# Kernel optimization log

Measured on AMD Instinct MI355X. Metric: run time of the kernel, lower is better.

The kernel has to match this reference:

```python
import jax, jax.numpy as jnp
import numpy as np

OBS = 4096      # flattened observation size (hardcoded in down_sampler)
ENC = 1024      # encoding_size
LAT = 512       # policy_latent_size
ACT = 3         # action_space_n
B = 4096        # batch
NMAX = 8        # max neighbors (padded ragged dim)


def setup_inputs() -> dict:
    key = jax.random.key(0)
    ks = jax.random.split(key, 16)

    def w(i, shape, fan_in):
        return jax.random.normal(ks[i], shape, jnp.float32) * (1.0 / np.sqrt(fan_in))

    return {
        "observation": jax.random.normal(ks[0], (B, OBS), jnp.float32),
        "neighbors": jax.random.normal(ks[1], (B, NMAX, LAT), jnp.float32),
        "neighbor_counts": jax.random.randint(ks[2], (B,), 0, 9, jnp.int32),
        # down_sampler: Linear(4096, ENC) + ReLU
        "W_ds": w(3, (ENC, OBS), OBS), "b_ds": jnp.zeros((ENC,), jnp.float32),
        # policy: Linear(ENC, LAT) + ReLU
        "W_pol": w(4, (LAT, ENC), ENC), "b_pol": jnp.zeros((LAT,), jnp.float32),
        # v_net: Linear(ENC, 1) + Tanh
        "W_v": w(5, (1, ENC), ENC), "b_v": jnp.zeros((1,), jnp.float32),
        # GRUCell(LAT, LAT): weight_ih [3L, L], weight_hh [3L, L]
        "W_ih": w(6, (3 * LAT, LAT), LAT), "b_ih": jnp.zeros((3 * LAT,), jnp.float32),
        "W_hh": w(7, (3 * LAT, LAT), LAT), "b_hh": jnp.zeros((3 * LAT,), jnp.float32),
        # to_probs: Linear(LAT, ACT) + ReLU + Softmax
        "W_pr": w(8, (ACT, LAT), LAT), "b_pr": jnp.zeros((ACT,), jnp.float32),
    }


def _gru_cell(x, h, W_ih, b_ih, W_hh, b_hh):
    # PyTorch GRUCell semantics; gates ordered (r, z, n)
    gi = x @ W_ih.T + b_ih          # [B, 3L]
    gh = h @ W_hh.T + b_hh          # [B, 3L]
    i_r, i_z, i_n = jnp.split(gi, 3, axis=-1)
    h_r, h_z, h_n = jnp.split(gh, 3, axis=-1)
    r = jax.nn.sigmoid(i_r + h_r)
    z = jax.nn.sigmoid(i_z + h_z)
    n = jnp.tanh(i_n + r * h_n)
    return (1.0 - z) * n + z * h


def reference(observation, neighbors, neighbor_counts,
              W_ds, b_ds, W_pol, b_pol, W_v, b_v,
              W_ih, b_ih, W_hh, b_hh, W_pr, b_pr):
    # step 0: forward_initial
    enc = jax.nn.relu(observation @ W_ds.T + b_ds)        # [B, ENC]
    pol = jax.nn.relu(enc @ W_pol.T + b_pol)              # [B, LAT]
    state_vals = jnp.tanh(enc @ W_v.T + b_v)              # [B, 1]

    # step 1: forward_communicate -- ragged GRU recurrence over padded neighbors
    xs = jnp.swapaxes(neighbors, 0, 1)                    # [NMAX, B, LAT]
    ts = jnp.arange(NMAX)

    def step(h, xt):
        x, t = xt
        h_new = _gru_cell(x, h, W_ih, b_ih, W_hh, b_hh)
        valid = (t < neighbor_counts)[:, None]            # mask padded neighbor slots
        return jnp.where(valid, h_new, h), None

    h, _ = jax.lax.scan(step, pol, (xs, ts))              # [B, LAT]

    # step 2: forward_probs
    probs = jax.nn.softmax(jax.nn.relu(h @ W_pr.T + b_pr), axis=-1)  # [B, ACT]
    return probs, state_vals
```

## Files before the change

### kernel.cpp

```cpp
#include <hip/hip_runtime.h>
#include <hip/hip_bf16.h>

typedef __attribute__((ext_vector_type(8))) short short8;
typedef __attribute__((ext_vector_type(4))) float floatx4;

__device__ __forceinline__ ushort f2bf(float x) {
    unsigned u = __float_as_uint(x);
    unsigned r = (u + 0x7fffu + ((u >> 16) & 1u)) >> 16;
    return (ushort)r;
}
__device__ __forceinline__ float bf2f(ushort h) {
    return __uint_as_float(((unsigned)h) << 16);
}
__device__ __forceinline__ float fast_sigmoid(float x) {
    return 1.0f / (1.0f + __expf(-x));
}
__device__ __forceinline__ float fast_tanh(float x) {
    x = fminf(fmaxf(x, -15.0f), 15.0f);
    float e = __expf(2.0f * x);
    return (e - 1.0f) / (e + 1.0f);
}
__device__ __forceinline__ void load_lds16(const void* g, void* l) {
    __builtin_amdgcn_global_load_lds(
        (__attribute__((address_space(1))) void*)(g),
        (__attribute__((address_space(3))) void*)(l),
        16, 0, 0);
}

__device__ __forceinline__ void stage_unit(const ushort* grow0, int ld, ushort* lds_unit) {
    const int lane = threadIdx.x & 63;
    const int r = lane >> 3;
    const int c = (lane & 7) ^ r;
    load_lds16(grow0 + (size_t)r * ld + c * 8, lds_unit);
}
__device__ __forceinline__ short8 lds_read8(const ushort* buf, int R, int c_el) {
    const int idx = ((R >> 3) << 9) + ((R & 7) << 6) + ((((c_el >> 3) ^ (R & 7))) << 3);
    return *(const short8*)(buf + idx);
}

__global__ __launch_bounds__(256) void cvt_f32_bf16(const float* __restrict__ src,
                                                    ushort* __restrict__ dst, int n4) {
    int i = blockIdx.x * blockDim.x + threadIdx.x;
    if (i >= n4) return;
    const float4 v = ((const float4*)src)[i];
    ushort4 o;
    o.x = f2bf(v.x); o.y = f2bf(v.y); o.z = f2bf(v.z); o.w = f2bf(v.w);
    ((ushort4*)dst)[i] = o;
}

__global__ __launch_bounds__(256) void sort_by_cnt(const int* __restrict__ cnt,
                                                   int* __restrict__ perm,
                                                   int* __restrict__ inv,
                                                   int* __restrict__ nact) {
    __shared__ int h[9];
    __shared__ int cur[9];
    const int tid = threadIdx.x;
    if (tid < 9) h[tid] = 0;
    __syncthreads();
    for (int i = tid; i < 4096; i += 256) atomicAdd(&h[cnt[i]], 1);
    __syncthreads();
    if (tid == 0) {
        int off = 0;
        for (int c = 8; c >= 0; --c) { cur[c] = off; off += h[c]; }
        for (int t = 0; t < 8; ++t) {
            int n = 0;
            for (int c = t + 1; c <= 8; ++c) n += h[c];
            nact[t] = n;
        }
    }
    __syncthreads();
    for (int i = tid; i < 4096; i += 256) {
        const int c = cnt[i];
        const int p = atomicAdd(&cur[c], 1);
        perm[p] = i;
        inv[i] = p;
    }
}

template <int MODE, int BN, int KSPLIT, bool MAP>
__global__ __launch_bounds__(256, 2) void gemm64(
    const ushort* __restrict__ A, int lda,
    const ushort* __restrict__ B, int ldb,
    const float* __restrict__ bias,
    const int* __restrict__ row_map,
    ushort* __restrict__ Cb, float* __restrict__ Cf, int ldc,
    int K, size_t part_stride) {
    __shared__ __attribute__((aligned(16))) ushort sA[64 * 64];
    __shared__ __attribute__((aligned(16))) ushort sB[BN * 64];

    constexpr int NJ = (BN + 63) / 64;
    constexpr int UB = BN / 32;

    const int tid = threadIdx.x;
    const int lane = tid & 63;
    const int w = tid >> 6;
    const int m0 = blockIdx.y * 64;
    const int n0 = blockIdx.x * BN;
    const int wn = w * (16 * NJ);
    const int nl = lane & 15;

    const int Kper = K / KSPLIT;
    const int kbase = (KSPLIT > 1) ? blockIdx.z * Kper : 0;
    if (MODE == 3) Cf += (size_t)blockIdx.z * part_stride;

    floatx4 acc[4][NJ] = {};

    for (int k0 = kbase; k0 < kbase + Kper; k0 += 64) {
#pragma unroll
        for (int u = 0; u < 2; ++u) {
            const int ua = w * 2 + u;
            stage_unit(A + (size_t)(m0 + ua * 8) * lda + k0, lda, &sA[ua * 512]);
        }
#pragma unroll
        for (int u = 0; u < UB; ++u) {
            const int ub = w * UB + u;
            stage_unit(B + (size_t)(n0 + ub * 8) * ldb + k0, ldb, &sB[ub * 512]);
        }
        __syncthreads();
#pragma unroll
        for (int kk = 0; kk < 2; ++kk) {
            const int cb = kk * 32 + (lane >> 4) * 8;
            short8 a[4], b[NJ];
#pragma unroll
            for (int i = 0; i < 4; ++i) a[i] = lds_read8(sA, i * 16 + nl, cb);
#pragma unroll
            for (int j = 0; j < NJ; ++j) b[j] = lds_read8(sB, wn + j * 16 + nl, cb);
#pragma unroll
            for (int i = 0; i < 4; ++i)
#pragma unroll
                for (int j = 0; j < NJ; ++j)
                    acc[i][j] = __builtin_amdgcn_mfma_f32_16x16x32_bf16(a[i], b[j], acc[i][j], 0, 0, 0);
        }
        __syncthreads();
    }

    const int ml = (lane >> 4) * 4;
#pragma unroll
    for (int j = 0; j < NJ; ++j) {
        const int n = n0 + wn + j * 16 + nl;
        float bv = 0.0f;
        if (MODE == 2) bv = bias[n];
#pragma unroll
        for (int i = 0; i < 4; ++i) {
            const int mbase = m0 + i * 16 + ml;
#pragma unroll
            for (int r = 0; r < 4; ++r) {
                float v = acc[i][j][r];
                const int mr = mbase + r;
                const int orow = MAP ? row_map[mr] : mr;
                const size_t off = (size_t)orow * ldc + n;
                if (MODE == 2) {
                    v += bv; v = fmaxf(v, 0.0f);
                    Cb[off] = f2bf(v);
                    Cf[off] = v;
                } else {
                    Cf[off] = v;
                }
            }
        }
    }
}

__global__ __launch_bounds__(256) void combine_relu(const float* __restrict__ p0,
                                                    const float* __restrict__ p1,
                                                    const float* __restrict__ bias,
                                                    ushort* __restrict__ ob, int n4) {
    int i = blockIdx.x * blockDim.x + threadIdx.x;
    if (i >= n4) return;
    const float4 a = ((const float4*)p0)[i];
    const float4 b = ((const float4*)p1)[i];
    const int col = (i * 4) & 1023;
    const float4 bs = *(const float4*)(bias + col);
    ushort4 o;
    o.x = f2bf(fmaxf(a.x + b.x + bs.x, 0.f));
    o.y = f2bf(fmaxf(a.y + b.y + bs.y, 0.f));
    o.z = f2bf(fmaxf(a.z + b.z + bs.z, 0.f));
    o.w = f2bf(fmaxf(a.w + b.w + bs.w, 0.f));
    ((ushort4*)ob)[i] = o;
}

__global__ __launch_bounds__(256, 2) void gru_step(
    const ushort* __restrict__ Xall,
    const ushort* __restrict__ Hin,
    const ushort* __restrict__ Wih,
    const ushort* __restrict__ Whh,
    const float* __restrict__ bih, const float* __restrict__ bhh,
    const int* __restrict__ perm, const int* __restrict__ nact,
    float* __restrict__ hf, ushort* __restrict__ Hout, int t) {
    __shared__ __attribute__((aligned(16))) ushort sX[64 * 64];
    __shared__ __attribute__((aligned(16))) ushort sH[64 * 64];
    __shared__ __attribute__((aligned(16))) ushort sBih[192 * 64];
    __shared__ __attribute__((aligned(16))) ushort sBhh[192 * 64];

    const int tid = threadIdx.x;
    const int lane = tid & 63;
    const int w = tid >> 6;
    const int s = blockIdx.x;
    const int m0 = blockIdx.y * 64;
    const int na = nact[t];

    if (m0 >= na) {
        const int rr = tid >> 2;
        const size_t base = (size_t)(m0 + rr) * 512 + s * 64;
        const uint4* src = (const uint4*)(Hin + base);
        uint4* dst = (uint4*)(Hout + base);
        const int cc = (tid & 3) * 2;
        dst[cc] = src[cc];
        dst[cc + 1] = src[cc + 1];
        return;
    }

    const int nl = lane & 15;
    const int ml = (lane >> 4) * 4;
    const int col = s * 64 + w * 16 + nl;

    const int r = lane >> 3;
    const int c = (lane & 7) ^ r;
    const ushort* X = Xall + t * 512;
    const ushort* xb[2];
    const ushort* hbp[2];
#pragma unroll
    for (int u = 0; u < 2; ++u) {
        const int srow = m0 + (w * 2 + u) * 8 + r;
        const int orig = perm[srow];
        xb[u] = X + (size_t)orig * 4096 + c * 8;
        hbp[u] = Hin + (size_t)srow * 512 + c * 8;
    }
    const ushort* wi[6];
    const ushort* wh[6];
#pragma unroll
    for (int j = 0; j < 6; ++j) {
        const int u = w * 6 + j;
        const int grow = (u >> 3) * 512 + s * 64 + (u & 7) * 8 + r;
        wi[j] = Wih + (size_t)grow * 512 + c * 8;
        wh[j] = Whh + (size_t)grow * 512 + c * 8;
    }

    floatx4 accr[4], accz[4], accn[4], acch[4];
    {
        const float br_ = bih[col] + bhh[col];
        const float bz_ = bih[512 + col] + bhh[512 + col];
        const float bn_i = bih[1024 + col];
        const float bn_h = bhh[1024 + col];
        const floatx4 vr = {br_, br_, br_, br_};
        const floatx4 vz = {bz_, bz_, bz_, bz_};
        const floatx4 vi = {bn_i, bn_i, bn_i, bn_i};
        const floatx4 vh = {bn_h, bn_h, bn_h, bn_h};
#pragma unroll
        for (int i = 0; i < 4; ++i) { accr[i] = vr; accz[i] = vz; accn[i] = vi; acch[i] = vh; }
    }

    for (int k0 = 0; k0 < 512; k0 += 64) {
#pragma unroll
        for (int u = 0; u < 2; ++u) {
            const int ua = w * 2 + u;
            load_lds16(xb[u] + k0, &sX[ua * 512]);
            load_lds16(hbp[u] + k0, &sH[ua * 512]);
        }
#pragma unroll
        for (int j = 0; j < 6; ++j) {
            const int u = w * 6 + j;
            load_lds16(wi[j] + k0, &sBih[u * 512]);
            load_lds16(wh[j] + k0, &sBhh[u * 512]);
        }
        __syncthreads();
#pragma unroll
        for (int kk = 0; kk < 2; ++kk) {
            const int cb = kk * 32 + (lane >> 4) * 8;
            short8 ax[4], ah[4];
#pragma unroll
            for (int i = 0; i < 4; ++i) {
                ax[i] = lds_read8(sX, i * 16 + nl, cb);
                ah[i] = lds_read8(sH, i * 16 + nl, cb);
            }
            const short8 bir = lds_read8(sBih, w * 16 + nl, cb);
            const short8 biz = lds_read8(sBih, 64 + w * 16 + nl, cb);
            const short8 bin = lds_read8(sBih, 128 + w * 16 + nl, cb);
            const short8 bhr = lds_read8(sBhh, w * 16 + nl, cb);
            const short8 bhz = lds_read8(sBhh, 64 + w * 16 + nl, cb);
            const short8 bhn = lds_read8(sBhh, 128 + w * 16 + nl, cb);
#pragma unroll
            for (int i = 0; i < 4; ++i) {
                accr[i] = __builtin_amdgcn_mfma_f32_16x16x32_bf16(ax[i], bir, accr[i], 0, 0, 0);
                accr[i] = __builtin_amdgcn_mfma_f32_16x16x32_bf16(ah[i], bhr, accr[i], 0, 0, 0);
                accz[i] = __builtin_amdgcn_mfma_f32_16x16x32_bf16(ax[i], biz, accz[i], 0, 0, 0);
                accz[i] = __builtin_amdgcn_mfma_f32_16x16x32_bf16(ah[i], bhz, accz[i], 0, 0, 0);
                accn[i] = __builtin_amdgcn_mfma_f32_16x16x32_bf16(ax[i], bin, accn[i], 0, 0, 0);
                acch[i] = __builtin_amdgcn_mfma_f32_16x16x32_bf16(ah[i], bhn, acch[i], 0, 0, 0);
            }
        }
        __syncthreads();
    }

    const bool full = (m0 + 64 <= na);
#pragma unroll
    for (int i = 0; i < 4; ++i) {
#pragma unroll
        for (int r4 = 0; r4 < 4; ++r4) {
            const int lr = i * 16 + ml + r4;
            const int row = m0 + lr;
            const float rg = fast_sigmoid(accr[i][r4]);
            const float zg = fast_sigmoid(accz[i][r4]);
            const float ng = fast_tanh(accn[i][r4] + rg * acch[i][r4]);
            const size_t off = (size_t)row * 512 + col;
            const float ho = hf[off];
            const bool act = full || (row < na);
            const float hv = act ? ((1.0f - zg) * ng + zg * ho) : ho;
            hf[off] = hv;
            Hout[off] = f2bf(hv);
        }
    }
}

__global__ __launch_bounds__(256) void v_kernel(const ushort* __restrict__ enc,
                                                const float* __restrict__ Wv,
                                                const float* __restrict__ bv,
                                                float* __restrict__ out) {
    const int row = blockIdx.x * 4 + (threadIdx.x >> 6);
    const int lane = threadIdx.x & 63;
    const ushort* e = enc + (size_t)row * 1024;
    float s = 0.0f;
#pragma unroll
    for (int i = 0; i < 16; ++i) {
        int k = lane + i * 64;
        s += bf2f(e[k]) * Wv[k];
    }
#pragma unroll
    for (int off = 32; off; off >>= 1) s += __shfl_down(s, off, 64);
    if (lane == 0) out[row] = fast_tanh(s + bv[0]);
}

__global__ __launch_bounds__(256) void probs_kernel(const float* __restrict__ h,
                                                    const float* __restrict__ Wpr,
                                                    const float* __restrict__ bpr,
                                                    const int* __restrict__ perm,
                                                    float* __restrict__ out) {
    const int srow = blockIdx.x * 4 + (threadIdx.x >> 6);
    const int lane = threadIdx.x & 63;
    const float* hr = h + (size_t)srow * 512;
    float p0 = 0.f, p1 = 0.f, p2 = 0.f;
#pragma unroll
    for (int i = 0; i < 8; ++i) {
        int k = lane + i * 64;
        float x = hr[k];
        p0 += x * Wpr[k];
        p1 += x * Wpr[512 + k];
        p2 += x * Wpr[1024 + k];
    }
#pragma unroll
    for (int off = 32; off; off >>= 1) {
        p0 += __shfl_down(p0, off, 64);
        p1 += __shfl_down(p1, off, 64);
        p2 += __shfl_down(p2, off, 64);
    }
    if (lane == 0) {
        const int orow = perm[srow];
        p0 = fmaxf(p0 + bpr[0], 0.f);
        p1 = fmaxf(p1 + bpr[1], 0.f);
        p2 = fmaxf(p2 + bpr[2], 0.f);
        float m = fmaxf(p0, fmaxf(p1, p2));
        float e0 = __expf(p0 - m), e1 = __expf(p1 - m), e2 = __expf(p2 - m);
        float inv = 1.0f / (e0 + e1 + e2);
        out[orow * 3 + 0] = e0 * inv;
        out[orow * 3 + 1] = e1 * inv;
        out[orow * 3 + 2] = e2 * inv;
    }
}

extern "C" void kernel_launch(void* const* d_in, const int* in_sizes, int n_in,
                              void* d_out, int out_size, void* d_ws, size_t ws_size,
                              hipStream_t stream) {
    const float* obs   = (const float*)d_in[0];
    const float* nbr   = (const float*)d_in[1];
    const int*   cnt   = (const int*)d_in[2];
    const float* W_ds  = (const float*)d_in[3];
    const float* b_ds  = (const float*)d_in[4];
    const float* W_pol = (const float*)d_in[5];
    const float* b_pol = (const float*)d_in[6];
    const float* W_v   = (const float*)d_in[7];
    const float* b_v   = (const float*)d_in[8];
    const float* W_ih  = (const float*)d_in[9];
    const float* b_ih  = (const float*)d_in[10];
    const float* W_hh  = (const float*)d_in[11];
    const float* b_hh  = (const float*)d_in[12];
    const float* W_pr  = (const float*)d_in[13];
    const float* b_pr  = (const float*)d_in[14];
    float* out = (float*)d_out;

    ushort* obs_b  = (ushort*)d_ws;
    ushort* Wds_b  = obs_b + 16777216;
    ushort* Wpol_b = Wds_b + 4194304;
    ushort* Wih_b  = Wpol_b + 524288;
    ushort* Whh_b  = Wih_b + 786432;
    ushort* enc_b  = Whh_b + 786432;
    ushort* h_b0   = enc_b + 4194304;
    ushort* h_b1   = h_b0 + 2097152;
    float*  h_f    = (float*)(h_b1 + 2097152);
    float*  part   = h_f + 2097152;
    ushort* nbr_b  = (ushort*)part;
    int*    perm   = (int*)(part + 8388608);
    int*    inv    = perm + 4096;
    int*    nact   = inv + 4096;

    sort_by_cnt<<<1, 256, 0, stream>>>(cnt, perm, inv, nact);

    cvt_f32_bf16<<<16384, 256, 0, stream>>>(obs, obs_b, 4194304);
    cvt_f32_bf16<<<4096, 256, 0, stream>>>(W_ds, Wds_b, 1048576);
    cvt_f32_bf16<<<512, 256, 0, stream>>>(W_pol, Wpol_b, 131072);
    cvt_f32_bf16<<<768, 256, 0, stream>>>(W_ih, Wih_b, 196608);
    cvt_f32_bf16<<<768, 256, 0, stream>>>(W_hh, Whh_b, 196608);

    gemm64<3, 128, 2, false><<<dim3(8, 64, 2), 256, 0, stream>>>(
        obs_b, 4096, Wds_b, 4096, nullptr, nullptr, nullptr, part, 1024, 4096, 4194304);
    combine_relu<<<4096, 256, 0, stream>>>(part, part + 4194304, b_ds, enc_b, 1048576);

    cvt_f32_bf16<<<16384, 256, 0, stream>>>(nbr, nbr_b, 4194304);

    gemm64<2, 64, 1, true><<<dim3(8, 64, 1), 256, 0, stream>>>(
        enc_b, 1024, Wpol_b, 1024, b_pol, inv, h_b0, h_f, 512, 1024, 0);

    v_kernel<<<1024, 256, 0, stream>>>(enc_b, W_v, b_v, out + 12288);

    for (int t = 0; t < 8; ++t) {
        const ushort* hin = (t & 1) ? h_b1 : h_b0;
        ushort* hout = (t & 1) ? h_b0 : h_b1;
        gru_step<<<dim3(8, 64), 256, 0, stream>>>(nbr_b, hin, Wih_b, Whh_b,
                                                  b_ih, b_hh, perm, nact, h_f, hout, t);
    }

    probs_kernel<<<1024, 256, 0, stream>>>(h_f, W_pr, b_pr, perm, out);
}
```

Measured before the change: 445.6 us.

## Double-buffer LDS and read weight fragments directly from global in GEMM and GRU

Adds a new down-sampler GEMM kernel with 128x256 tiles that double-buffers only the A tile in LDS and loads B (weight) fragments straight from global memory into registers. The GRU step kernel is changed the same way: X/H tiles are double-buffered with one barrier per K step, and W_ih/W_hh fragments are loaded per lane from global instead of being staged in LDS. The goal is to overlap loads with MFMA, cut barriers, and shrink LDS use. The cost is uncoalesced global weight reads that now depend on the cache, plus higher register pressure from the 8x4 accumulator tile.

```diff
diff --git a/kernel.cpp b/kernel.cpp
--- a/kernel.cpp
+++ b/kernel.cpp
@@ -27,15 +27,15 @@
         16, 0, 0);
 }
 
+__device__ __forceinline__ short8 lds_read8(const ushort* buf, int R, int c_el) {
+    const int idx = ((R >> 3) << 9) + ((R & 7) << 6) + ((((c_el >> 3) ^ (R & 7))) << 3);
+    return *(const short8*)(buf + idx);
+}
 __device__ __forceinline__ void stage_unit(const ushort* grow0, int ld, ushort* lds_unit) {
     const int lane = threadIdx.x & 63;
     const int r = lane >> 3;
     const int c = (lane & 7) ^ r;
     load_lds16(grow0 + (size_t)r * ld + c * 8, lds_unit);
-}
-__device__ __forceinline__ short8 lds_read8(const ushort* buf, int R, int c_el) {
-    const int idx = ((R >> 3) << 9) + ((R & 7) << 6) + ((((c_el >> 3) ^ (R & 7))) << 3);
-    return *(const short8*)(buf + idx);
 }
 
 __global__ __launch_bounds__(256) void cvt_f32_bf16(const float* __restrict__ src,
@@ -77,14 +77,92 @@
     }
 }
 
-template <int MODE, int BN, int KSPLIT, bool MAP>
+template <int KSPLIT>
+__global__ __launch_bounds__(256, 2) void gemm_bigm(
+    const ushort* __restrict__ A, int lda,
+    const ushort* __restrict__ B, int ldb,
+    float* __restrict__ Cf, int ldc, int K, size_t part_stride) {
+    __shared__ __attribute__((aligned(16))) ushort sA[2][128 * 64];
+
+    const int tid = threadIdx.x;
+    const int lane = tid & 63;
+    const int w = tid >> 6;
+    const int m0 = blockIdx.y * 128;
+    const int n0 = blockIdx.x * 256;
+    const int nl = lane & 15;
+    const int wcol = (lane >> 4) * 8;
+
+    const int Kper = K / KSPLIT;
+    const int kbase = blockIdx.z * Kper;
+    Cf += (size_t)blockIdx.z * part_stride;
+
+    const int r = lane >> 3;
+    const int c = (lane & 7) ^ r;
+    const ushort* ab[4];
+#pragma unroll
+    for (int u = 0; u < 4; ++u) {
+        const int ua = w * 4 + u;
+        ab[u] = A + (size_t)(m0 + ua * 8 + r) * lda + kbase + c * 8;
+    }
+    const ushort* bp[4];
+#pragma unroll
+    for (int j = 0; j < 4; ++j)
+        bp[j] = B + (size_t)(n0 + w * 64 + j * 16 + nl) * ldb + kbase + wcol;
+
+    floatx4 acc[8][4] = {};
+
+#pragma unroll
+    for (int u = 0; u < 4; ++u) load_lds16(ab[u], &sA[0][(w * 4 + u) * 512]);
+
+    const int iters = Kper / 64;
+    for (int it = 0; it < iters; ++it) {
+        const int cur = it & 1;
+        __syncthreads();
+        if (it + 1 < iters) {
+            const int kn = (it + 1) * 64;
+#pragma unroll
+            for (int u = 0; u < 4; ++u) load_lds16(ab[u] + kn, &sA[cur ^ 1][(w * 4 + u) * 512]);
+        }
+        const int k0 = it * 64;
+#pragma unroll
+        for (int kk = 0; kk < 2; ++kk) {
+            const int kc = k0 + kk * 32;
+            short8 b[4];
+#pragma unroll
+            for (int j = 0; j < 4; ++j) b[j] = *(const short8*)(bp[j] + kc);
+            const int cb = kk * 32 + wcol;
+            short8 a[8];
+#pragma unroll
+            for (int i = 0; i < 8; ++i) a[i] = lds_read8(&sA[cur][0], i * 16 + nl, cb);
+#pragma unroll
+            for (int i = 0; i < 8; ++i)
+#pragma unroll
+                for (int j = 0; j < 4; ++j)
+                    acc[i][j] = __builtin_amdgcn_mfma_f32_16x16x32_bf16(a[i], b[j], acc[i][j], 0, 0, 0);
+        }
+    }
+
+    const int ml = (lane >> 4) * 4;
+#pragma unroll
+    for (int j = 0; j < 4; ++j) {
+        const int n = n0 + w * 64 + j * 16 + nl;
+#pragma unroll
+        for (int i = 0; i < 8; ++i) {
+            const int mbase = m0 + i * 16 + ml;
+#pragma unroll
+            for (int r4 = 0; r4 < 4; ++r4)
+                Cf[(size_t)(mbase + r4) * ldc + n] = acc[i][j][r4];
+        }
+    }
+}
+
+template <int MODE, int BN, bool MAP>
 __global__ __launch_bounds__(256, 2) void gemm64(
     const ushort* __restrict__ A, int lda,
     const ushort* __restrict__ B, int ldb,
     const float* __restrict__ bias,
     const int* __restrict__ row_map,
-    ushort* __restrict__ Cb, float* __restrict__ Cf, int ldc,
-    int K, size_t part_stride) {
+    ushort* __restrict__ Cb, float* __restrict__ Cf, int ldc, int K) {
     __shared__ __attribute__((aligned(16))) ushort sA[64 * 64];
     __shared__ __attribute__((aligned(16))) ushort sB[BN * 64];
 
@@ -99,13 +177,9 @@
     const int wn = w * (16 * NJ);
     const int nl = lane & 15;
 
-    const int Kper = K / KSPLIT;
-    const int kbase = (KSPLIT > 1) ? blockIdx.z * Kper : 0;
-    if (MODE == 3) Cf += (size_t)blockIdx.z * part_stride;
-
     floatx4 acc[4][NJ] = {};
 
-    for (int k0 = kbase; k0 < kbase + Kper; k0 += 64) {
+    for (int k0 = 0; k0 < K; k0 += 64) {
 #pragma unroll
         for (int u = 0; u < 2; ++u) {
             const int ua = w * 2 + u;
@@ -138,8 +212,7 @@
 #pragma unroll
     for (int j = 0; j < NJ; ++j) {
         const int n = n0 + wn + j * 16 + nl;
-        float bv = 0.0f;
-        if (MODE == 2) bv = bias[n];
+        const float bv = bias[n];
 #pragma unroll
         for (int i = 0; i < 4; ++i) {
             const int mbase = m0 + i * 16 + ml;
@@ -149,13 +222,9 @@
                 const int mr = mbase + r;
                 const int orow = MAP ? row_map[mr] : mr;
                 const size_t off = (size_t)orow * ldc + n;
-                if (MODE == 2) {
-                    v += bv; v = fmaxf(v, 0.0f);
-                    Cb[off] = f2bf(v);
-                    Cf[off] = v;
-                } else {
-                    Cf[off] = v;
-                }
+                v += bv; v = fmaxf(v, 0.0f);
+                Cb[off] = f2bf(v);
+                Cf[off] = v;
             }
         }
     }
@@ -187,10 +256,8 @@
     const float* __restrict__ bih, const float* __restrict__ bhh,
     const int* __restrict__ perm, const int* __restrict__ nact,
     float* __restrict__ hf, ushort* __restrict__ Hout, int t) {
-    __shared__ __attribute__((aligned(16))) ushort sX[64 * 64];
-    __shared__ __attribute__((aligned(16))) ushort sH[64 * 64];
-    __shared__ __attribute__((aligned(16))) ushort sBih[192 * 64];
-    __shared__ __attribute__((aligned(16))) ushort sBhh[192 * 64];
+    __shared__ __attribute__((aligned(16))) ushort sX[2][64 * 64];
+    __shared__ __attribute__((aligned(16))) ushort sH[2][64 * 64];
 
     const int tid = threadIdx.x;
     const int lane = tid & 63;
@@ -212,6 +279,7 @@
 
     const int nl = lane & 15;
     const int ml = (lane >> 4) * 4;
+    const int wcol = (lane >> 4) * 8;
     const int col = s * 64 + w * 16 + nl;
 
     const int r = lane >> 3;
@@ -222,74 +290,80 @@
 #pragma unroll
     for (int u = 0; u < 2; ++u) {
         const int srow = m0 + (w * 2 + u) * 8 + r;
-        const int orig = perm[srow];
-        xb[u] = X + (size_t)orig * 4096 + c * 8;
+        xb[u] = X + (size_t)perm[srow] * 4096 + c * 8;
         hbp[u] = Hin + (size_t)srow * 512 + c * 8;
     }
-    const ushort* wi[6];
-    const ushort* wh[6];
-#pragma unroll
-    for (int j = 0; j < 6; ++j) {
-        const int u = w * 6 + j;
-        const int grow = (u >> 3) * 512 + s * 64 + (u & 7) * 8 + r;
-        wi[j] = Wih + (size_t)grow * 512 + c * 8;
-        wh[j] = Whh + (size_t)grow * 512 + c * 8;
-    }
+    const ushort* pir = Wih + (size_t)col * 512 + wcol;
+    const ushort* piz = Wih + (size_t)(512 + col) * 512 + wcol;
+    const ushort* pin = Wih + (size_t)(1024 + col) * 512 + wcol;
+    const ushort* phr = Whh + (size_t)col * 512 + wcol;
+    const ushort* phz = Whh + (size_t)(512 + col) * 512 + wcol;
+    const ushort* phn = Whh + (size_t)(1024 + col) * 512 + wcol;
 
     floatx4 accr[4], accz[4], accn[4], acch[4];
     {
         const float br_ = bih[col] + bhh[col];
         const float bz_ = bih[512 + col] + bhh[512 + col];
-        const float bn_i = bih[1024 + col];
-        const float bn_h = bhh[1024 + col];
+        const float bni = bih[1024 + col];
+        const float bnh = bhh[1024 + col];
         const floatx4 vr = {br_, br_, br_, br_};
         const floatx4 vz = {bz_, bz_, bz_, bz_};
-        const floatx4 vi = {bn_i, bn_i, bn_i, bn_i};
-        const floatx4 vh = {bn_h, bn_h, bn_h, bn_h};
+        const floatx4 vi = {bni, bni, bni, bni};
+        const floatx4 vh = {bnh, bnh, bnh, bnh};
 #pragma unroll
         for (int i = 0; i < 4; ++i) { accr[i] = vr; accz[i] = vz; accn[i] = vi; acch[i] = vh; }
     }
 
-    for (int k0 = 0; k0 < 512; k0 += 64) {
-#pragma unroll
-        for (int u = 0; u < 2; ++u) {
-            const int ua = w * 2 + u;
-            load_lds16(xb[u] + k0, &sX[ua * 512]);
-            load_lds16(hbp[u] + k0, &sH[ua * 512]);
-        }
-#pragma unroll
-        for (int j = 0; j < 6; ++j) {
-            const int u = w * 6 + j;
-            load_lds16(wi[j] + k0, &sBih[u * 512]);
-            load_lds16(wh[j] + k0, &sBhh[u * 512]);
-        }
+#pragma unroll
+    for (int u = 0; u < 2; ++u) {
+        const int ua = w * 2 + u;
+        load_lds16(xb[u], &sX[0][ua * 512]);
+        load_lds16(hbp[u], &sH[0][ua * 512]);
+    }
+
+    for (int it = 0; it < 8; ++it) {
+        const int cur = it & 1;
         __syncthreads();
+        if (it < 7) {
+            const int kn = (it + 1) * 64;
+#pragma unroll
+            for (int u = 0; u < 2; ++u) {
+                const int ua = w * 2 + u;
+                load_lds16(xb[u] + kn, &sX[cur ^ 1][ua * 512]);
+                load_lds16(hbp[u] + kn, &sH[cur ^ 1][ua * 512]);
+            }
+        }
+        const int k0 = it * 64;
+        short8 wf[12];
 #pragma unroll
         for (int kk = 0; kk < 2; ++kk) {
-            const int cb = kk * 32 + (lane >> 4) * 8;
+            const int kc = k0 + kk * 32;
+            wf[kk * 6 + 0] = *(const short8*)(pir + kc);
+            wf[kk * 6 + 1] = *(const short8*)(piz + kc);
+            wf[kk * 6 + 2] = *(const short8*)(pin + kc);
+            wf[kk * 6 + 3] = *(const short8*)(phr + kc);
+            wf[kk * 6 + 4] = *(const short8*)(phz + kc);
+            wf[kk * 6 + 5] = *(const short8*)(phn + kc);
+        }
+#pragma unroll
+        for (int kk = 0; kk < 2; ++kk) {
+            const int cb = kk * 32 + wcol;
             short8 ax[4], ah[4];
 #pragma unroll
             for (int i = 0; i < 4; ++i) {
-                ax[i] = lds_read8(sX, i * 16 + nl, cb);
-                ah[i] = lds_read8(sH, i * 16 + nl, cb);
+                ax[i] = lds_read8(&sX[cur][0], i * 16 + nl, cb);
+                ah[i] = lds_read8(&sH[cur][0], i * 16 + nl, cb);
             }
-            const short8 bir = lds_read8(sBih, w * 16 + nl, cb);
-            const short8 biz = lds_read8(sBih, 64 + w * 16 + nl, cb);
-            const short8 bin = lds_read8(sBih, 128 + w * 16 + nl, cb);
-            const short8 bhr = lds_read8(sBhh, w * 16 + nl, cb);
-            const short8 bhz = lds_read8(sBhh, 64 + w * 16 + nl, cb);
-            const short8 bhn = lds_read8(sBhh, 128 + w * 16 + nl, cb);
 #pragma unroll
             for (int i = 0; i < 4; ++i) {
-                accr[i] = __builtin_amdgcn_mfma_f32_16x16x32_bf16(ax[i], bir, accr[i], 0, 0, 0);
-                accr[i] = __builtin_amdgcn_mfma_f32_16x16x32_bf16(ah[i], bhr, accr[i], 0, 0, 0);
-                accz[i] = __builtin_amdgcn_mfma_f32_16x16x32_bf16(ax[i], biz, accz[i], 0, 0, 0);
-                accz[i] = __builtin_amdgcn_mfma_f32_16x16x32_bf16(ah[i], bhz, accz[i], 0, 0, 0);
-                accn[i] = __builtin_amdgcn_mfma_f32_16x16x32_bf16(ax[i], bin, accn[i], 0, 0, 0);
-                acch[i] = __builtin_amdgcn_mfma_f32_16x16x32_bf16(ah[i], bhn, acch[i], 0, 0, 0);
+                accr[i] = __builtin_amdgcn_mfma_f32_16x16x32_bf16(ax[i], wf[kk * 6 + 0], accr[i], 0, 0, 0);
+                accr[i] = __builtin_amdgcn_mfma_f32_16x16x32_bf16(ah[i], wf[kk * 6 + 3], accr[i], 0, 0, 0);
+                accz[i] = __builtin_amdgcn_mfma_f32_16x16x32_bf16(ax[i], wf[kk * 6 + 1], accz[i], 0, 0, 0);
+                accz[i] = __builtin_amdgcn_mfma_f32_16x16x32_bf16(ah[i], wf[kk * 6 + 4], accz[i], 0, 0, 0);
+                accn[i] = __builtin_amdgcn_mfma_f32_16x16x32_bf16(ax[i], wf[kk * 6 + 2], accn[i], 0, 0, 0);
+                acch[i] = __builtin_amdgcn_mfma_f32_16x16x32_bf16(ah[i], wf[kk * 6 + 5], acch[i], 0, 0, 0);
             }
         }
-        __syncthreads();
     }
 
     const bool full = (m0 + 64 <= na);
@@ -297,8 +371,7 @@
     for (int i = 0; i < 4; ++i) {
 #pragma unroll
         for (int r4 = 0; r4 < 4; ++r4) {
-            const int lr = i * 16 + ml + r4;
-            const int row = m0 + lr;
+            const int row = m0 + i * 16 + ml + r4;
             const float rg = fast_sigmoid(accr[i][r4]);
             const float zg = fast_sigmoid(accz[i][r4]);
             const float ng = fast_tanh(accn[i][r4] + rg * acch[i][r4]);
@@ -410,14 +483,14 @@
     cvt_f32_bf16<<<768, 256, 0, stream>>>(W_ih, Wih_b, 196608);
     cvt_f32_bf16<<<768, 256, 0, stream>>>(W_hh, Whh_b, 196608);
 
-    gemm64<3, 128, 2, false><<<dim3(8, 64, 2), 256, 0, stream>>>(
-        obs_b, 4096, Wds_b, 4096, nullptr, nullptr, nullptr, part, 1024, 4096, 4194304);
+    gemm_bigm<2><<<dim3(4, 32, 2), 256, 0, stream>>>(
+        obs_b, 4096, Wds_b, 4096, part, 1024, 4096, 4194304);
     combine_relu<<<4096, 256, 0, stream>>>(part, part + 4194304, b_ds, enc_b, 1048576);
 
     cvt_f32_bf16<<<16384, 256, 0, stream>>>(nbr, nbr_b, 4194304);
 
-    gemm64<2, 64, 1, true><<<dim3(8, 64, 1), 256, 0, stream>>>(
-        enc_b, 1024, Wpol_b, 1024, b_pol, inv, h_b0, h_f, 512, 1024, 0);
+    gemm64<2, 64, true><<<dim3(8, 64), 256, 0, stream>>>(
+        enc_b, 1024, Wpol_b, 1024, b_pol, inv, h_b0, h_f, 512, 1024);
 
     v_kernel<<<1024, 256, 0, stream>>>(enc_b, W_v, b_v, out + 12288);
 
```

Measured after the change: 529.0 us. 18.7% more time.

## Retile GRU step to 128-row tiles with double-buffered LDS and register weights

Applied to the files above, without the earlier changes.

The GRU step kernel now covers 128 batch rows per block instead of 64, with the grid reordered to (M tiles, column slices). X and H tiles are double-buffered in LDS so the next K chunk's global-to-LDS copies overlap the current MFMAs, and one barrier per iteration replaces two. Weight fragments are read straight from global memory into registers rather than staged through LDS. This is meant to amortise the weight traffic over more rows and hide load latency. In exchange it launches fewer blocks, roughly doubles accumulator registers (launch bound lowered to one block per SIMD set), and exposes global-load latency on the weight reads.

```diff
diff --git a/kernel.cpp b/kernel.cpp
--- a/kernel.cpp
+++ b/kernel.cpp
@@ -27,15 +27,15 @@
         16, 0, 0);
 }
 
+__device__ __forceinline__ short8 lds_read8(const ushort* buf, int R, int c_el) {
+    const int idx = ((R >> 3) << 9) + ((R & 7) << 6) + ((((c_el >> 3) ^ (R & 7))) << 3);
+    return *(const short8*)(buf + idx);
+}
 __device__ __forceinline__ void stage_unit(const ushort* grow0, int ld, ushort* lds_unit) {
     const int lane = threadIdx.x & 63;
     const int r = lane >> 3;
     const int c = (lane & 7) ^ r;
     load_lds16(grow0 + (size_t)r * ld + c * 8, lds_unit);
-}
-__device__ __forceinline__ short8 lds_read8(const ushort* buf, int R, int c_el) {
-    const int idx = ((R >> 3) << 9) + ((R & 7) << 6) + ((((c_el >> 3) ^ (R & 7))) << 3);
-    return *(const short8*)(buf + idx);
 }
 
 __global__ __launch_bounds__(256) void cvt_f32_bf16(const float* __restrict__ src,
@@ -179,7 +179,7 @@
     ((ushort4*)ob)[i] = o;
 }
 
-__global__ __launch_bounds__(256, 2) void gru_step(
+__global__ __launch_bounds__(256, 1) void gru_step(
     const ushort* __restrict__ Xall,
     const ushort* __restrict__ Hin,
     const ushort* __restrict__ Wih,
@@ -187,100 +187,102 @@
     const float* __restrict__ bih, const float* __restrict__ bhh,
     const int* __restrict__ perm, const int* __restrict__ nact,
     float* __restrict__ hf, ushort* __restrict__ Hout, int t) {
-    __shared__ __attribute__((aligned(16))) ushort sX[64 * 64];
-    __shared__ __attribute__((aligned(16))) ushort sH[64 * 64];
-    __shared__ __attribute__((aligned(16))) ushort sBih[192 * 64];
-    __shared__ __attribute__((aligned(16))) ushort sBhh[192 * 64];
+    __shared__ __attribute__((aligned(16))) ushort sX[2][128 * 64];
+    __shared__ __attribute__((aligned(16))) ushort sH[2][128 * 64];
 
     const int tid = threadIdx.x;
     const int lane = tid & 63;
     const int w = tid >> 6;
-    const int s = blockIdx.x;
-    const int m0 = blockIdx.y * 64;
+    const int m0 = blockIdx.x * 128;
+    const int s = blockIdx.y;
     const int na = nact[t];
 
     if (m0 >= na) {
-        const int rr = tid >> 2;
+        const int rr = tid >> 1;
         const size_t base = (size_t)(m0 + rr) * 512 + s * 64;
         const uint4* src = (const uint4*)(Hin + base);
         uint4* dst = (uint4*)(Hout + base);
-        const int cc = (tid & 3) * 2;
-        dst[cc] = src[cc];
-        dst[cc + 1] = src[cc + 1];
+        const int cc = (tid & 1) * 4;
+#pragma unroll
+        for (int q = 0; q < 4; ++q) dst[cc + q] = src[cc + q];
         return;
     }
 
     const int nl = lane & 15;
     const int ml = (lane >> 4) * 4;
+    const int wcol = (lane >> 4) * 8;
     const int col = s * 64 + w * 16 + nl;
 
     const int r = lane >> 3;
     const int c = (lane & 7) ^ r;
     const ushort* X = Xall + t * 512;
-    const ushort* xb[2];
-    const ushort* hbp[2];
-#pragma unroll
-    for (int u = 0; u < 2; ++u) {
-        const int srow = m0 + (w * 2 + u) * 8 + r;
-        const int orig = perm[srow];
-        xb[u] = X + (size_t)orig * 4096 + c * 8;
-        hbp[u] = Hin + (size_t)srow * 512 + c * 8;
-    }
-    const ushort* wi[6];
-    const ushort* wh[6];
-#pragma unroll
-    for (int j = 0; j < 6; ++j) {
-        const int u = w * 6 + j;
-        const int grow = (u >> 3) * 512 + s * 64 + (u & 7) * 8 + r;
-        wi[j] = Wih + (size_t)grow * 512 + c * 8;
-        wh[j] = Whh + (size_t)grow * 512 + c * 8;
-    }
-
-    floatx4 accr[4], accz[4], accn[4], acch[4];
+    const ushort* xb[4];
+    const ushort* hb[4];
+#pragma unroll
+    for (int u = 0; u < 4; ++u) {
+        const int srow = m0 + (w * 4 + u) * 8 + r;
+        xb[u] = X + (size_t)perm[srow] * 4096 + c * 8;
+        hb[u] = Hin + (size_t)srow * 512 + c * 8;
+    }
+    const ushort* pir = Wih + (size_t)col * 512 + wcol;
+    const ushort* piz = Wih + (size_t)(512 + col) * 512 + wcol;
+    const ushort* pin = Wih + (size_t)(1024 + col) * 512 + wcol;
+    const ushort* phr = Whh + (size_t)col * 512 + wcol;
+    const ushort* phz = Whh + (size_t)(512 + col) * 512 + wcol;
+    const ushort* phn = Whh + (size_t)(1024 + col) * 512 + wcol;
+
+    floatx4 accr[8], accz[8], accn[8], acch[8];
     {
         const float br_ = bih[col] + bhh[col];
         const float bz_ = bih[512 + col] + bhh[512 + col];
-        const float bn_i = bih[1024 + col];
-        const float bn_h = bhh[1024 + col];
+        const float bni = bih[1024 + col];
+        const float bnh = bhh[1024 + col];
         const floatx4 vr = {br_, br_, br_, br_};
         const floatx4 vz = {bz_, bz_, bz_, bz_};
-        const floatx4 vi = {bn_i, bn_i, bn_i, bn_i};
-        const floatx4 vh = {bn_h, bn_h, bn_h, bn_h};
-#pragma unroll
-        for (int i = 0; i < 4; ++i) { accr[i] = vr; accz[i] = vz; accn[i] = vi; acch[i] = vh; }
-    }
-
-    for (int k0 = 0; k0 < 512; k0 += 64) {
-#pragma unroll
-        for (int u = 0; u < 2; ++u) {
-            const int ua = w * 2 + u;
-            load_lds16(xb[u] + k0, &sX[ua * 512]);
-            load_lds16(hbp[u] + k0, &sH[ua * 512]);
-        }
-#pragma unroll
-        for (int j = 0; j < 6; ++j) {
-            const int u = w * 6 + j;
-            load_lds16(wi[j] + k0, &sBih[u * 512]);
-            load_lds16(wh[j] + k0, &sBhh[u * 512]);
-        }
+        const floatx4 vi = {bni, bni, bni, bni};
+        const floatx4 vh = {bnh, bnh, bnh, bnh};
+#pragma unroll
+        for (int i = 0; i < 8; ++i) { accr[i] = vr; accz[i] = vz; accn[i] = vi; acch[i] = vh; }
+    }
+
+#pragma unroll
+    for (int u = 0; u < 4; ++u) {
+        const int ua = w * 4 + u;
+        load_lds16(xb[u], &sX[0][ua * 512]);
+        load_lds16(hb[u], &sH[0][ua * 512]);
+    }
+
+    for (int it = 0; it < 8; ++it) {
+        const int cur = it & 1;
         __syncthreads();
+        if (it < 7) {
+            const int kn = (it + 1) * 64;
+#pragma unroll
+            for (int u = 0; u < 4; ++u) {
+                const int ua = w * 4 + u;
+                load_lds16(xb[u] + kn, &sX[cur ^ 1][ua * 512]);
+                load_lds16(hb[u] + kn, &sH[cur ^ 1][ua * 512]);
+            }
+        }
+        const int k0 = it * 64;
 #pragma unroll
         for (int kk = 0; kk < 2; ++kk) {
-            const int cb = kk * 32 + (lane >> 4) * 8;
-            short8 ax[4], ah[4];
-#pragma unroll
-            for (int i = 0; i < 4; ++i) {
-                ax[i] = lds_read8(sX, i * 16 + nl, cb);
-                ah[i] = lds_read8(sH, i * 16 + nl, cb);
+            const int kc = k0 + kk * 32;
+            const short8 bir = *(const short8*)(pir + kc);
+            const short8 biz = *(const short8*)(piz + kc);
+            const short8 bin = *(const short8*)(pin + kc);
+            const short8 bhr = *(const short8*)(phr + kc);
+            const short8 bhz = *(const short8*)(phz + kc);
+            const short8 bhn = *(const short8*)(phn + kc);
+            const int cb = kk * 32 + wcol;
+            short8 ax[8], ah[8];
+#pragma unroll
+            for (int i = 0; i < 8; ++i) {
+                ax[i] = lds_read8(&sX[cur][0], i * 16 + nl, cb);
+                ah[i] = lds_read8(&sH[cur][0], i * 16 + nl, cb);
             }
-            const short8 bir = lds_read8(sBih, w * 16 + nl, cb);
-            const short8 biz = lds_read8(sBih, 64 + w * 16 + nl, cb);
-            const short8 bin = lds_read8(sBih, 128 + w * 16 + nl, cb);
-            const short8 bhr = lds_read8(sBhh, w * 16 + nl, cb);
-            const short8 bhz = lds_read8(sBhh, 64 + w * 16 + nl, cb);
-            const short8 bhn = lds_read8(sBhh, 128 + w * 16 + nl, cb);
-#pragma unroll
-            for (int i = 0; i < 4; ++i) {
+#pragma unroll
+            for (int i = 0; i < 8; ++i) {
                 accr[i] = __builtin_amdgcn_mfma_f32_16x16x32_bf16(ax[i], bir, accr[i], 0, 0, 0);
                 accr[i] = __builtin_amdgcn_mfma_f32_16x16x32_bf16(ah[i], bhr, accr[i], 0, 0, 0);
                 accz[i] = __builtin_amdgcn_mfma_f32_16x16x32_bf16(ax[i], biz, accz[i], 0, 0, 0);
@@ -289,16 +291,14 @@
                 acch[i] = __builtin_amdgcn_mfma_f32_16x16x32_bf16(ah[i], bhn, acch[i], 0, 0, 0);
             }
         }
-        __syncthreads();
-    }
-
-    const bool full = (m0 + 64 <= na);
-#pragma unroll
-    for (int i = 0; i < 4; ++i) {
+    }
+
+    const bool full = (m0 + 128 <= na);
+#pragma unroll
+    for (int i = 0; i < 8; ++i) {
 #pragma unroll
         for (int r4 = 0; r4 < 4; ++r4) {
-            const int lr = i * 16 + ml + r4;
-            const int row = m0 + lr;
+            const int row = m0 + i * 16 + ml + r4;
             const float rg = fast_sigmoid(accr[i][r4]);
             const float zg = fast_sigmoid(accz[i][r4]);
             const float ng = fast_tanh(accn[i][r4] + rg * acch[i][r4]);
@@ -424,7 +424,7 @@
     for (int t = 0; t < 8; ++t) {
         const ushort* hin = (t & 1) ? h_b1 : h_b0;
         ushort* hout = (t & 1) ? h_b0 : h_b1;
-        gru_step<<<dim3(8, 64), 256, 0, stream>>>(nbr_b, hin, Wih_b, Whh_b,
+        gru_step<<<dim3(32, 8), 256, 0, stream>>>(nbr_b, hin, Wih_b, Whh_b,
                                                   b_ih, b_hh, perm, nact, h_f, hout, t);
     }
 
```

Result: slower. 594.2 us (+33.4%).

## Load GRU operands directly from global into registers with double buffering

Applied to the files above, without the earlier changes.

The GRU step kernel no longer stages X, H and weight tiles through LDS with barriers. Each lane now loads its MFMA fragments straight from global memory into registers, using a two-deep register prefetch over the K dimension. This removes LDS traffic and __syncthreads, but it gives up sharing across the four waves, so each activation fragment is loaded by every wave, and it raises register pressure.

```diff
diff --git a/kernel.cpp b/kernel.cpp
--- a/kernel.cpp
+++ b/kernel.cpp
@@ -27,15 +27,15 @@
         16, 0, 0);
 }
 
+__device__ __forceinline__ short8 lds_read8(const ushort* buf, int R, int c_el) {
+    const int idx = ((R >> 3) << 9) + ((R & 7) << 6) + ((((c_el >> 3) ^ (R & 7))) << 3);
+    return *(const short8*)(buf + idx);
+}
 __device__ __forceinline__ void stage_unit(const ushort* grow0, int ld, ushort* lds_unit) {
     const int lane = threadIdx.x & 63;
     const int r = lane >> 3;
     const int c = (lane & 7) ^ r;
     load_lds16(grow0 + (size_t)r * ld + c * 8, lds_unit);
-}
-__device__ __forceinline__ short8 lds_read8(const ushort* buf, int R, int c_el) {
-    const int idx = ((R >> 3) << 9) + ((R & 7) << 6) + ((((c_el >> 3) ^ (R & 7))) << 3);
-    return *(const short8*)(buf + idx);
 }
 
 __global__ __launch_bounds__(256) void cvt_f32_bf16(const float* __restrict__ src,
@@ -187,11 +187,6 @@
     const float* __restrict__ bih, const float* __restrict__ bhh,
     const int* __restrict__ perm, const int* __restrict__ nact,
     float* __restrict__ hf, ushort* __restrict__ Hout, int t) {
-    __shared__ __attribute__((aligned(16))) ushort sX[64 * 64];
-    __shared__ __attribute__((aligned(16))) ushort sH[64 * 64];
-    __shared__ __attribute__((aligned(16))) ushort sBih[192 * 64];
-    __shared__ __attribute__((aligned(16))) ushort sBhh[192 * 64];
-
     const int tid = threadIdx.x;
     const int lane = tid & 63;
     const int w = tid >> 6;
@@ -212,84 +207,71 @@
 
     const int nl = lane & 15;
     const int ml = (lane >> 4) * 4;
+    const int qk = (lane >> 4) * 8;
     const int col = s * 64 + w * 16 + nl;
 
-    const int r = lane >> 3;
-    const int c = (lane & 7) ^ r;
     const ushort* X = Xall + t * 512;
-    const ushort* xb[2];
-    const ushort* hbp[2];
-#pragma unroll
-    for (int u = 0; u < 2; ++u) {
-        const int srow = m0 + (w * 2 + u) * 8 + r;
-        const int orig = perm[srow];
-        xb[u] = X + (size_t)orig * 4096 + c * 8;
-        hbp[u] = Hin + (size_t)srow * 512 + c * 8;
-    }
-    const ushort* wi[6];
-    const ushort* wh[6];
-#pragma unroll
-    for (int j = 0; j < 6; ++j) {
-        const int u = w * 6 + j;
-        const int grow = (u >> 3) * 512 + s * 64 + (u & 7) * 8 + r;
-        wi[j] = Wih + (size_t)grow * 512 + c * 8;
-        wh[j] = Whh + (size_t)grow * 512 + c * 8;
-    }
+    const ushort* xb[4];
+    const ushort* hb[4];
+#pragma unroll
+    for (int mt = 0; mt < 4; ++mt) {
+        const int srow = m0 + mt * 16 + nl;
+        xb[mt] = X + (size_t)perm[srow] * 4096 + qk;
+        hb[mt] = Hin + (size_t)srow * 512 + qk;
+    }
+    const ushort* wb[6];
+    wb[0] = Wih + (size_t)col * 512 + qk;
+    wb[1] = Wih + (size_t)(512 + col) * 512 + qk;
+    wb[2] = Wih + (size_t)(1024 + col) * 512 + qk;
+    wb[3] = Whh + (size_t)col * 512 + qk;
+    wb[4] = Whh + (size_t)(512 + col) * 512 + qk;
+    wb[5] = Whh + (size_t)(1024 + col) * 512 + qk;
 
     floatx4 accr[4], accz[4], accn[4], acch[4];
     {
         const float br_ = bih[col] + bhh[col];
         const float bz_ = bih[512 + col] + bhh[512 + col];
-        const float bn_i = bih[1024 + col];
-        const float bn_h = bhh[1024 + col];
+        const float bni = bih[1024 + col];
+        const float bnh = bhh[1024 + col];
         const floatx4 vr = {br_, br_, br_, br_};
         const floatx4 vz = {bz_, bz_, bz_, bz_};
-        const floatx4 vi = {bn_i, bn_i, bn_i, bn_i};
-        const floatx4 vh = {bn_h, bn_h, bn_h, bn_h};
+        const floatx4 vi = {bni, bni, bni, bni};
+        const floatx4 vh = {bnh, bnh, bnh, bnh};
 #pragma unroll
         for (int i = 0; i < 4; ++i) { accr[i] = vr; accz[i] = vz; accn[i] = vi; acch[i] = vh; }
     }
 
-    for (int k0 = 0; k0 < 512; k0 += 64) {
-#pragma unroll
-        for (int u = 0; u < 2; ++u) {
-            const int ua = w * 2 + u;
-            load_lds16(xb[u] + k0, &sX[ua * 512]);
-            load_lds16(hbp[u] + k0, &sH[ua * 512]);
-        }
-#pragma unroll
-        for (int j = 0; j < 6; ++j) {
-            const int u = w * 6 + j;
-            load_lds16(wi[j] + k0, &sBih[u * 512]);
-            load_lds16(wh[j] + k0, &sBhh[u * 512]);
-        }
-        __syncthreads();
-#pragma unroll
-        for (int kk = 0; kk < 2; ++kk) {
-            const int cb = kk * 32 + (lane >> 4) * 8;
-            short8 ax[4], ah[4];
-#pragma unroll
-            for (int i = 0; i < 4; ++i) {
-                ax[i] = lds_read8(sX, i * 16 + nl, cb);
-                ah[i] = lds_read8(sH, i * 16 + nl, cb);
+    short8 fx[2][4], fh[2][4], fw[2][6];
+#pragma unroll
+    for (int mt = 0; mt < 4; ++mt) {
+        fx[0][mt] = *(const short8*)(xb[mt]);
+        fh[0][mt] = *(const short8*)(hb[mt]);
+    }
+#pragma unroll
+    for (int g = 0; g < 6; ++g) fw[0][g] = *(const short8*)(wb[g]);
+
+    for (int ck = 0; ck < 16; ++ck) {
+        const int cur = ck & 1;
+        const int nxt = cur ^ 1;
+        if (ck < 15) {
+            const int kc = (ck + 1) * 32;
+#pragma unroll
+            for (int mt = 0; mt < 4; ++mt) {
+                fx[nxt][mt] = *(const short8*)(xb[mt] + kc);
+                fh[nxt][mt] = *(const short8*)(hb[mt] + kc);
             }
-            const short8 bir = lds_read8(sBih, w * 16 + nl, cb);
-            const short8 biz = lds_read8(sBih, 64 + w * 16 + nl, cb);
-            const short8 bin = lds_read8(sBih, 128 + w * 16 + nl, cb);
-            const short8 bhr = lds_read8(sBhh, w * 16 + nl, cb);
-            const short8 bhz = lds_read8(sBhh, 64 + w * 16 + nl, cb);
-            const short8 bhn = lds_read8(sBhh, 128 + w * 16 + nl, cb);
-#pragma unroll
-            for (int i = 0; i < 4; ++i) {
-                accr[i] = __builtin_amdgcn_mfma_f32_16x16x32_bf16(ax[i], bir, accr[i], 0, 0, 0);
-                accr[i] = __builtin_amdgcn_mfma_f32_16x16x32_bf16(ah[i], bhr, accr[i], 0, 0, 0);
-                accz[i] = __builtin_amdgcn_mfma_f32_16x16x32_bf16(ax[i], biz, accz[i], 0, 0, 0);
-                accz[i] = __builtin_amdgcn_mfma_f32_16x16x32_bf16(ah[i], bhz, accz[i], 0, 0, 0);
-                accn[i] = __builtin_amdgcn_mfma_f32_16x16x32_bf16(ax[i], bin, accn[i], 0, 0, 0);
-                acch[i] = __builtin_amdgcn_mfma_f32_16x16x32_bf16(ah[i], bhn, acch[i], 0, 0, 0);
-            }
-        }
-        __syncthreads();
+#pragma unroll
+            for (int g = 0; g < 6; ++g) fw[nxt][g] = *(const short8*)(wb[g] + kc);
+        }
+#pragma unroll
+        for (int i = 0; i < 4; ++i) {
+            accr[i] = __builtin_amdgcn_mfma_f32_16x16x32_bf16(fx[cur][i], fw[cur][0], accr[i], 0, 0, 0);
+            accr[i] = __builtin_amdgcn_mfma_f32_16x16x32_bf16(fh[cur][i], fw[cur][3], accr[i], 0, 0, 0);
+            accz[i] = __builtin_amdgcn_mfma_f32_16x16x32_bf16(fx[cur][i], fw[cur][1], accz[i], 0, 0, 0);
+            accz[i] = __builtin_amdgcn_mfma_f32_16x16x32_bf16(fh[cur][i], fw[cur][4], accz[i], 0, 0, 0);
+            accn[i] = __builtin_amdgcn_mfma_f32_16x16x32_bf16(fx[cur][i], fw[cur][2], accn[i], 0, 0, 0);
+            acch[i] = __builtin_amdgcn_mfma_f32_16x16x32_bf16(fh[cur][i], fw[cur][5], acch[i], 0, 0, 0);
+        }
     }
 
     const bool full = (m0 + 64 <= na);
@@ -297,8 +279,7 @@
     for (int i = 0; i < 4; ++i) {
 #pragma unroll
         for (int r4 = 0; r4 < 4; ++r4) {
-            const int lr = i * 16 + ml + r4;
-            const int row = m0 + lr;
+            const int row = m0 + i * 16 + ml + r4;
             const float rg = fast_sigmoid(accr[i][r4]);
             const float zg = fast_sigmoid(accz[i][r4]);
             const float ng = fast_tanh(accn[i][r4] + rg * acch[i][r4]);
```

Result: slower. 677.4 us (+52.0%).
